# Kernel optimization log

Hardware: AMD Instinct MI355X
Metric: run time of the kernel (lower is better)

## Reference

```python
import jax, jax.numpy as jnp
import numpy as np

V_THRESHOLD = 1.0
V_RESET = 0.0
TAU = 2.0
SURROGATE_PARAM = 0.5  # 'zo' (rectangular window) surrogate half-width


@jax.custom_vjp
def act_fun(x):
    # Heaviside step: spike if membrane exceeds threshold
    return (x > 0).astype(x.dtype)


def _act_fwd(x):
    return act_fun(x), x


def _act_bwd(x, g):
    # zero-order / rectangular surrogate gradient:
    # d spike / dx = 1/(2a) * 1[|x| < a]
    a = SURROGATE_PARAM
    grad = g * (jnp.abs(x) < a).astype(g.dtype) / (2.0 * a)
    return (grad,)


act_fun.defvjp(_act_fwd, _act_bwd)


def lif_forward(X):
    # X: [B, T, N] -> spikes [B, T, N]
    Xt = jnp.swapaxes(X, 0, 1)  # [T, B, N]

    def step(mem, x_t):
        # leaky integration toward (input + v_reset)
        mem = mem + (x_t + V_RESET - mem) / TAU
        spike = act_fun(mem - V_THRESHOLD)
        # hard reset to v_reset where spiked
        mem = (1.0 - spike) * mem + V_RESET * spike
        return mem, spike

    mem0 = jnp.zeros(Xt.shape[1:], dtype=X.dtype)
    _, spikes = jax.lax.scan(step, mem0, Xt)  # spikes: [T, B, N]
    return jnp.swapaxes(spikes, 0, 1)  # [B, T, N]


def setup_inputs() -> dict:
    key = jax.random.key(0)
    B, T, N = 128, 32, 8192
    X = jax.random.normal(key, (B, T, N), dtype=jnp.float32)
    return {"X": X}


def reference(X):
    return lif_forward(X)
```

## Files before the change

### kernel.cpp

```cpp
#include <hip/hip_runtime.h>


#define T_STEPS 32
#define N2 4096
#define TN2 (T_STEPS * N2)

__global__ __launch_bounds__(256) void lif_fwd_kernel(
    const float2* __restrict__ X, float2* __restrict__ out)
{
    const int idx = blockIdx.x * blockDim.x + threadIdx.x;
    const int b = idx >> 12;
    const int n = idx & (N2 - 1);
    const size_t base = (size_t)b * (size_t)TN2 + (size_t)n;

    const float2* p = X + base;
    float2* __restrict__ po = out + base;

    float2 x[T_STEPS];
#pragma unroll
    for (int t = 0; t < T_STEPS; ++t) {
        asm volatile("global_load_dwordx2 %0, %1, off"
                     : "=v"(x[t])
                     : "v"(p));
        p += N2;
    }

    asm volatile("s_waitcnt vmcnt(0)" ::: "memory");

#pragma unroll
    for (int t = 0; t < T_STEPS; ++t)
        asm volatile("" : "+v"(x[t]));

    float m0 = 0.f, m1 = 0.f;
#pragma unroll
    for (int t = 0; t < T_STEPS; ++t) {
        m0 = m0 + (x[t].x - m0) * 0.5f;
        m1 = m1 + (x[t].y - m1) * 0.5f;

        float2 s;
        s.x = (m0 - 1.0f > 0.0f) ? 1.0f : 0.0f;
        s.y = (m1 - 1.0f > 0.0f) ? 1.0f : 0.0f;

        m0 = (s.x != 0.0f) ? 0.0f : m0;
        m1 = (s.y != 0.0f) ? 0.0f : m1;

        po[(size_t)t * (size_t)N2] = s;
    }
}

extern "C" void kernel_launch(void* const* d_in, const int* in_sizes, int n_in,
                              void* d_out, int out_size, void* d_ws, size_t ws_size,
                              hipStream_t stream) {
    const float2* X = (const float2*)d_in[0];
    float2* out = (float2*)d_out;

    const int total = in_sizes[0];
    const int B = total / (T_STEPS * 8192);
    const int nthreads = B * N2;

    const int block = 256;
    const int grid = (nthreads + block - 1) / block;

    lif_fwd_kernel<<<grid, block, 0, stream>>>(X, out);
}
```

Before: 224.2 us.

## Stagger wave start with sleeps, software-pipeline loads, use nontemporal stores

Drops the batched inline-asm loads of all 32 timesteps followed by a full vmcnt wait, and replaces them with a one-ahead prefetch loop in plain C so the compiler can schedule loads around the compute. Adds a per-wave s_sleep stagger keyed on wave and block index so waves desynchronise their memory bursts. Output stores become nontemporal to avoid polluting cache. The risk is that with only one load in flight per thread, memory-level parallelism may drop unless the compiler hoists more loads, and the sleeps add startup latency.

```diff
diff --git a/kernel.cpp b/kernel.cpp
--- a/kernel.cpp
+++ b/kernel.cpp
@@ -1,5 +1,7 @@
 #include <hip/hip_runtime.h>
 
+
+typedef float v2f __attribute__((ext_vector_type(2)));
 
 #define T_STEPS 32
 #define N2 4096
@@ -8,43 +10,44 @@
 __global__ __launch_bounds__(256) void lif_fwd_kernel(
     const float2* __restrict__ X, float2* __restrict__ out)
 {
+    {
+        const int slot = ((threadIdx.x >> 6) + ((blockIdx.x & 7) << 2)) & 31;
+        if (slot & 1)  __builtin_amdgcn_s_sleep(4);
+        if (slot & 2)  __builtin_amdgcn_s_sleep(8);
+        if (slot & 4)  __builtin_amdgcn_s_sleep(16);
+        if (slot & 8)  __builtin_amdgcn_s_sleep(32);
+        if (slot & 16) __builtin_amdgcn_s_sleep(64);
+    }
+
     const int idx = blockIdx.x * blockDim.x + threadIdx.x;
     const int b = idx >> 12;
     const int n = idx & (N2 - 1);
     const size_t base = (size_t)b * (size_t)TN2 + (size_t)n;
 
-    const float2* p = X + base;
-    float2* __restrict__ po = out + base;
+    const float2* __restrict__ px = X + base;
+    v2f* po = (v2f*)(out + base);
 
-    float2 x[T_STEPS];
+    float m0 = 0.f, m1 = 0.f;
+
+    float2 x = px[0];
+
 #pragma unroll
     for (int t = 0; t < T_STEPS; ++t) {
-        asm volatile("global_load_dwordx2 %0, %1, off"
-                     : "=v"(x[t])
-                     : "v"(p));
-        p += N2;
-    }
+        float2 xn;
+        if (t + 1 < T_STEPS) xn = px[(size_t)(t + 1) * (size_t)N2];
 
-    asm volatile("s_waitcnt vmcnt(0)" ::: "memory");
+        m0 = m0 + (x.x - m0) * 0.5f;
+        m1 = m1 + (x.y - m1) * 0.5f;
 
-#pragma unroll
-    for (int t = 0; t < T_STEPS; ++t)
-        asm volatile("" : "+v"(x[t]));
-
-    float m0 = 0.f, m1 = 0.f;
-#pragma unroll
-    for (int t = 0; t < T_STEPS; ++t) {
-        m0 = m0 + (x[t].x - m0) * 0.5f;
-        m1 = m1 + (x[t].y - m1) * 0.5f;
-
-        float2 s;
+        v2f s;
         s.x = (m0 - 1.0f > 0.0f) ? 1.0f : 0.0f;
         s.y = (m1 - 1.0f > 0.0f) ? 1.0f : 0.0f;
 
         m0 = (s.x != 0.0f) ? 0.0f : m0;
         m1 = (s.y != 0.0f) ? 0.0f : m1;
 
-        po[(size_t)t * (size_t)N2] = s;
+        __builtin_nontemporal_store(s, po + (size_t)t * (size_t)N2);
+        x = xn;
     }
 }
 
```

New measurement: 231.9 us. +3.4%, slower.
